# Kernel tuning notes

Measured on AMD Instinct MI355X. Metric: run time of the kernel, lower is better.

Reference implementation:

```python
import jax, jax.numpy as jnp
import numpy as np

B, L, H = 4, 1024, 1024          # docs, seq_len, hidden (LUKE-large)
NH, M, E, R = 16, 64, 24, 512    # attn heads, mentions/doc, entities/doc, pairs/doc
EMB, BLK, NCLS = 768, 64, 97     # embed_size, block_size, num_class


def setup_inputs() -> dict:
    key = jax.random.key(0)
    ks = jax.random.split(key, 10)
    s = 0.02
    return {
        "seq_lhs": jax.random.normal(ks[0], (B, L, H), jnp.float32),
        "ent_lhs": jax.random.normal(ks[1], (B, M, H), jnp.float32),
        "ent_to_seq_attn": jax.random.uniform(ks[2], (B, NH, M, L), jnp.float32),
        "entity_id_labels": jax.random.randint(ks[3], (B, M), 0, E),
        "hts": jax.random.randint(ks[4], (B, R, 2), 0, E),
        "Wh": jax.random.normal(ks[5], (2 * H, EMB), jnp.float32) * s,
        "bh": jnp.zeros((EMB,), jnp.float32),
        "Wt": jax.random.normal(ks[6], (2 * H, EMB), jnp.float32) * s,
        "bt": jnp.zeros((EMB,), jnp.float32),
        "Wb": jax.random.normal(ks[7], (EMB * BLK, 768), jnp.float32) * s,
        "bb": jnp.zeros((768,), jnp.float32),
        "Wc": jax.random.normal(ks[8], (768, NCLS), jnp.float32) * s,
        "bc": jnp.zeros((NCLS,), jnp.float32),
    }


def reference(seq_lhs, ent_lhs, ent_to_seq_attn, entity_id_labels, hts,
              Wh, bh, Wt, bt, Wb, bb, Wc, bc):
    dt = seq_lhs.dtype
    # mention -> entity segment mask [B, E, M]
    mask = entity_id_labels[:, None, :] == jnp.arange(E)[None, :, None]
    counts = mask.sum(-1)  # [B, E]
    # entity embedding: logsumexp over its mentions (== identity for 1 mention),
    # zeros for entities with no mentions
    masked = jnp.where(mask[..., None], ent_lhs[:, None, :, :], jnp.asarray(-1e30, dt))
    ent_emb = jax.scipy.special.logsumexp(masked, axis=2)           # [B, E, H]
    ent_emb = jnp.where((counts > 0)[..., None], ent_emb, jnp.asarray(0.0, dt))
    # entity -> seq attention: mean over mentions, zeros for empty entities
    mf = mask.astype(dt)
    ent_attn = jnp.einsum('bem,bhml->behl', mf, ent_to_seq_attn)    # [B, E, NH, L]
    ent_attn = ent_attn / jnp.maximum(counts, 1)[:, :, None, None].astype(dt)
    # gather per-pair head/tail embeddings and attentions
    h_idx, t_idx = hts[..., 0], hts[..., 1]                          # [B, R]
    hs = jnp.take_along_axis(ent_emb, h_idx[..., None], axis=1)      # [B, R, H]
    ts = jnp.take_along_axis(ent_emb, t_idx[..., None], axis=1)
    ha = jnp.take_along_axis(ent_attn, h_idx[..., None, None], axis=1)  # [B, R, NH, L]
    ta = jnp.take_along_axis(ent_attn, t_idx[..., None, None], axis=1)
    ht = (ha * ta).mean(2)                                           # [B, R, L]
    ht = ht / (ht.sum(-1, keepdims=True) + 1e-5)
    rel = jnp.einsum('bld,brl->brd', seq_lhs, ht)                    # [B, R, H]
    # head/tail extractors with context concat
    he = jnp.tanh(jnp.concatenate([hs, rel], -1) @ Wh + bh)          # [B, R, EMB]
    te = jnp.tanh(jnp.concatenate([ts, rel], -1) @ Wt + bt)
    K = EMB // BLK
    b1 = he.reshape(B * R, K, BLK)
    b2 = te.reshape(B * R, K, BLK)
    bl = (b1[:, :, :, None] * b2[:, :, None, :]).reshape(B * R, EMB * BLK)
    embeds = bl @ Wb + bb                                            # [B*R, 768]
    return embeds @ Wc + bc                                          # [B*R, NCLS]
```

## Files before the change

kernel.cpp:

```cpp
#include <hip/hip_runtime.h>
#include <stdint.h>
#include <math.h>

#define B_    4
#define L_    1024
#define H_    1024
#define NH_   16
#define M_    64
#define E_    24
#define R_    512
#define EMB_  768
#define BLK_  64
#define NCLS_ 97
#define NR_   2048
#define KBIG_ 49152

typedef unsigned short ushort_t;
typedef unsigned int uint_t;
typedef short bf16x8 __attribute__((ext_vector_type(8)));
typedef float f32x4  __attribute__((ext_vector_type(4)));
typedef __bf16 bf16v2 __attribute__((ext_vector_type(2)));

__device__ __forceinline__ float bf2f(ushort_t u) {
    return __uint_as_float(((unsigned)u) << 16);
}
__device__ __forceinline__ ushort_t f2bf_rne(float f) {
    unsigned u = __float_as_uint(f);
    return (ushort_t)((u + 0x7fffu + ((u >> 16) & 1u)) >> 16);
}
__device__ __forceinline__ void cp16(const void* g, void* l) {
    __builtin_amdgcn_global_load_lds(
        (const __attribute__((address_space(1))) void*)g,
        (__attribute__((address_space(3))) void*)l, 16, 0, 0);
}

__global__ __launch_bounds__(256) void k_transpose_cvt(
    const float* __restrict__ in, ushort_t* __restrict__ out, int rows, int cols)
{
    __shared__ float t[64][65];
    int batch = blockIdx.z;
    in  += (size_t)batch * rows * cols;
    out += (size_t)batch * rows * cols;
    int c0 = blockIdx.x * 64, r0 = blockIdx.y * 64;
    int tx = threadIdx.x & 63, ty = threadIdx.x >> 6;
#pragma unroll
    for (int dr = 0; dr < 64; dr += 4)
        t[dr + ty][tx] = in[(size_t)(r0 + dr + ty) * cols + (c0 + tx)];
    __syncthreads();
    int c = threadIdx.x >> 2;
    int rk = (threadIdx.x & 3) * 16;
    ushort_t us[16];
#pragma unroll
    for (int q = 0; q < 16; q++) us[q] = f2bf_rne(t[rk + q][c]);
    ushort_t* op = &out[(size_t)(c0 + c) * rows + r0 + rk];
    *reinterpret_cast<int4*>(op)     = *reinterpret_cast<const int4*>(&us[0]);
    *reinterpret_cast<int4*>(op + 8) = *reinterpret_cast<const int4*>(&us[8]);
}

__global__ __launch_bounds__(256) void k_ent_emb(
    const float* __restrict__ ent_lhs, const int* __restrict__ labels,
    float* __restrict__ ent_emb)
{
    int b = blockIdx.x / E_, e = blockIdx.x % E_;
    __shared__ int list[M_];
    __shared__ int cnt;
    if (threadIdx.x == 0) cnt = 0;
    __syncthreads();
    if (threadIdx.x < M_ && labels[b * M_ + threadIdx.x] == e) {
        int p = atomicAdd(&cnt, 1);
        list[p] = threadIdx.x;
    }
    __syncthreads();
    int n = cnt;
    const float* base = ent_lhs + (size_t)b * M_ * H_;
    float* outp = ent_emb + ((size_t)b * E_ + e) * H_;
    for (int h = threadIdx.x; h < H_; h += blockDim.x) {
        if (n == 0) { outp[h] = 0.f; continue; }
        float mx = -1e30f;
        for (int i = 0; i < n; i++) mx = fmaxf(mx, base[(size_t)list[i] * H_ + h]);
        float s = 0.f;
        for (int i = 0; i < n; i++) s += __expf(base[(size_t)list[i] * H_ + h] - mx);
        outp[h] = mx + __logf(s);
    }
}

__global__ __launch_bounds__(256) void k_ent_attn(
    const float* __restrict__ attn, const int* __restrict__ labels,
    float* __restrict__ ent_attn)
{
    int idx = blockIdx.x;
    int nh = idx % NH_;
    int be = idx / NH_;
    int e = be % E_, b = be / E_;
    __shared__ int list[M_];
    __shared__ int cnt;
    if (threadIdx.x == 0) cnt = 0;
    __syncthreads();
    if (threadIdx.x < M_ && labels[b * M_ + threadIdx.x] == e) {
        int p = atomicAdd(&cnt, 1);
        list[p] = threadIdx.x;
    }
    __syncthreads();
    int n = cnt;
    float inv = 1.f / fmaxf((float)n, 1.f);
    const float* base = attn + ((size_t)b * NH_ + nh) * M_ * L_;
    float* outp = ent_attn + (((size_t)b * E_ + e) * NH_ + nh) * L_;
    for (int l = threadIdx.x; l < L_; l += blockDim.x) {
        float s = 0.f;
        for (int i = 0; i < n; i++) s += base[(size_t)list[i] * L_ + l];
        outp[l] = s * inv;
    }
}

__global__ __launch_bounds__(256) void k_ht(
    const float* __restrict__ ent_attn, const int* __restrict__ hts,
    ushort_t* __restrict__ ht_bf)
{
    int b = blockIdx.x / R_, r = blockIdx.x % R_;
    int h = hts[((size_t)b * R_ + r) * 2 + 0];
    int t = hts[((size_t)b * R_ + r) * 2 + 1];
    const float* ha = ent_attn + ((size_t)b * E_ + h) * NH_ * L_;
    const float* ta = ent_attn + ((size_t)b * E_ + t) * NH_ * L_;
    float vals[4];
    float local = 0.f;
#pragma unroll
    for (int p = 0; p < 4; p++) {
        int l = threadIdx.x + p * 256;
        float s = 0.f;
#pragma unroll
        for (int nh = 0; nh < NH_; nh++) s += ha[nh * L_ + l] * ta[nh * L_ + l];
        s *= (1.f / NH_);
        vals[p] = s;
        local += s;
    }
    __shared__ float red[4];
    float s = local;
#pragma unroll
    for (int off = 32; off > 0; off >>= 1) s += __shfl_down(s, off, 64);
    if ((threadIdx.x & 63) == 0) red[threadIdx.x >> 6] = s;
    __syncthreads();
    float tot = red[0] + red[1] + red[2] + red[3];
    float inv = 1.f / (tot + 1e-5f);
    ushort_t* outp = ht_bf + ((size_t)b * R_ + r) * L_;
#pragma unroll
    for (int p = 0; p < 4; p++) {
        int l = threadIdx.x + p * 256;
        outp[l] = f2bf_rne(vals[p] * inv);
    }
}

__global__ __launch_bounds__(256) void k_gather(
    const float* __restrict__ ent_emb, const int* __restrict__ hts,
    ushort_t* __restrict__ A1, ushort_t* __restrict__ A2)
{
    int n = blockIdx.x;
    int b = n / R_, r = n % R_;
    int h = hts[((size_t)b * R_ + r) * 2 + 0];
    int t = hts[((size_t)b * R_ + r) * 2 + 1];
    const float* eh = ent_emb + ((size_t)b * E_ + h) * H_;
    const float* et = ent_emb + ((size_t)b * E_ + t) * H_;
    for (int i = threadIdx.x; i < H_; i += 256) {
        A1[(size_t)n * 2048 + i] = f2bf_rne(eh[i]);
        A2[(size_t)n * 2048 + i] = f2bf_rne(et[i]);
    }
}

template <bool BIAS, bool TANH, bool DUAL>
__global__ __launch_bounds__(256) void k_gemm(
    const ushort_t* __restrict__ A, long sA, int lda,
    const ushort_t* __restrict__ Bt, long sB, int ldb,
    int K,
    const float* __restrict__ bias0, const float* __restrict__ bias1,
    ushort_t* __restrict__ C0, ushort_t* __restrict__ C1, long sC, int ldc)
{
    __shared__ ushort_t smem[2 * 128 * 72];
    ushort_t* As = smem;
    ushort_t* Bs = smem + 128 * 72;
    const int tid = threadIdx.x;
    const int lane = tid & 63, wid = tid >> 6;
    const int wr = wid >> 1, wc = wid & 1;
    const int z = blockIdx.z;
    const int m0 = blockIdx.y * 128, n0 = blockIdx.x * 128;
    A  += (long)z * sA;
    Bt += (long)z * sB;

    const f32x4 zero = {0.f, 0.f, 0.f, 0.f};
    f32x4 acc[4][4];
#pragma unroll
    for (int i = 0; i < 4; i++)
#pragma unroll
        for (int j = 0; j < 4; j++) acc[i][j] = zero;

    const int mrow = wr * 64 + (lane & 15);
    const int nrow = wc * 64 + (lane & 15);
    const int koff = (lane >> 4) * 8;

    for (int k0 = 0; k0 < K; k0 += 64) {
        __syncthreads();
#pragma unroll
        for (int p = 0; p < 4; p++) {
            int idx = tid + p * 256;
            int row = idx >> 3, seg = idx & 7;
            *reinterpret_cast<int4*>(&As[row * 72 + seg * 8]) =
                *reinterpret_cast<const int4*>(&A[(long)(m0 + row) * lda + k0 + seg * 8]);
            *reinterpret_cast<int4*>(&Bs[row * 72 + seg * 8]) =
                *reinterpret_cast<const int4*>(&Bt[(long)(n0 + row) * ldb + k0 + seg * 8]);
        }
        __syncthreads();
#pragma unroll
        for (int ks = 0; ks < 2; ks++) {
            bf16x8 af[4], bfg[4];
#pragma unroll
            for (int mt = 0; mt < 4; mt++)
                af[mt] = *reinterpret_cast<const bf16x8*>(&As[(mrow + mt * 16) * 72 + ks * 32 + koff]);
#pragma unroll
            for (int nt = 0; nt < 4; nt++)
                bfg[nt] = *reinterpret_cast<const bf16x8*>(&Bs[(nrow + nt * 16) * 72 + ks * 32 + koff]);
#pragma unroll
            for (int mt = 0; mt < 4; mt++)
#pragma unroll
                for (int nt = 0; nt < 4; nt++)
                    acc[mt][nt] = __builtin_amdgcn_mfma_f32_16x16x32_bf16(
                        af[mt], bfg[nt], acc[mt][nt], 0, 0, 0);
        }
    }

    const float* bias = BIAS ? (z ? bias1 : bias0) : nullptr;
    __syncthreads();
#pragma unroll
    for (int mt = 0; mt < 4; mt++) {
#pragma unroll
        for (int nt = 0; nt < 4; nt++) {
#pragma unroll
            for (int rg = 0; rg < 4; rg++) {
                int row = wr * 64 + mt * 16 + (lane >> 4) * 4 + rg;
                int col = wc * 64 + nt * 16 + (lane & 15);
                float v = acc[mt][nt][rg];
                if (BIAS) v += bias[n0 + col];
                if (TANH) {
                    float vc = fminf(fmaxf(v, -15.f), 15.f);
                    float ex = __expf(2.f * vc);
                    v = (ex - 1.f) / (ex + 1.f);
                }
                smem[row * 132 + col] = f2bf_rne(v);
            }
        }
    }
    __syncthreads();
    {
        int row = tid >> 1, half = tid & 1;
        const ushort_t* src = &smem[row * 132 + half * 64];
        ushort_t* dst0 = &C0[(long)z * sC + (long)(m0 + row) * ldc + n0 + half * 64];
#pragma unroll
        for (int q = 0; q < 8; q++)
            *reinterpret_cast<int4*>(dst0 + q * 8) = *reinterpret_cast<const int4*>(src + q * 8);
        if (DUAL) {
            ushort_t* dst1 = &C1[(long)z * sC + (long)(m0 + row) * ldc + n0 + half * 64];
#pragma unroll
            for (int q = 0; q < 8; q++)
                *reinterpret_cast<int4*>(dst1 + q * 8) = *reinterpret_cast<const int4*>(src + q * 8);
        }
    }
}

__global__ __launch_bounds__(256, 3) void k_bilinear(
    const ushort_t* __restrict__ he, const ushort_t* __restrict__ te,
    const ushort_t* __restrict__ Wbt, float* __restrict__ embedsN, int slices)
{
    __shared__ ushort_t HEs[128 * 72];
    __shared__ ushort_t Bsh[128 * 64];
    const int tid = threadIdx.x;
    const int lane = tid & 63, wid = tid >> 6;
    const int wr = wid >> 1, wc = wid & 1;
    const int bid = blockIdx.x;
    const int z = bid & 7;
    const int w = bid >> 3;
    const int d0 = (w % 6) * 128, n0 = (w / 6) * 128;
    const int c0 = z * 96, cend = c0 + 96;

    const f32x4 zero = {0.f, 0.f, 0.f, 0.f};
    f32x4 acc[4][4];
#pragma unroll
    for (int i = 0; i < 4; i++)
#pragma unroll
        for (int j = 0; j < 4; j++) acc[i][j] = zero;

    const int r15 = lane & 15;
    const int q4 = lane >> 4;
    const int mrow = wr * 64 + r15;
    const int koff = q4 * 8;

    const ushort_t* Pg = Wbt
        + (long)(d0 + wid * 32 + (lane >> 3)) * KBIG_
        + ((lane & 7) ^ ((lane >> 3) & 7)) * 8;
    ushort_t* Pl = Bsh + wid * 2048;

    int c = c0;
    while (c < cend) {
        const int kk = c >> 6;
        const int i0 = c & 63;
        const int i1 = min(64, i0 + (cend - c));

        __syncthreads();
#pragma unroll
        for (int p = 0; p < 4; p++) {
            int idx = tid + p * 256;
            int row = idx >> 3, seg = idx & 7;
            *reinterpret_cast<int4*>(&HEs[row * 72 + seg * 8]) =
                *reinterpret_cast<const int4*>(&he[(long)(n0 + row) * EMB_ + kk * 64 + seg * 8]);
        }
        __syncthreads();

        uint4 tef[4][2];
#pragma unroll
        for (int mt = 0; mt < 4; mt++)
#pragma unroll
            for (int ks = 0; ks < 2; ks++)
                tef[mt][ks] = *reinterpret_cast<const uint4*>(
                    &te[(long)(n0 + mrow + mt * 16) * EMB_ + kk * 64 + ks * 32 + koff]);

        for (int i = i0; i < i1; i++) {
            const ushort_t* g = Pg + (long)(kk * 64 + i) * 64;
            cp16(g,              Pl);
            cp16(g +  8 * KBIG_, Pl + 512);
            cp16(g + 16 * KBIG_, Pl + 1024);
            cp16(g + 24 * KBIG_, Pl + 1536);
            __syncthreads();

#pragma unroll
            for (int ks = 0; ks < 2; ks++) {
                const int segoff = (((ks * 4 + q4) ^ (r15 & 7)) * 8);
                bf16x8 bfr[4];
#pragma unroll
                for (int nt = 0; nt < 4; nt++)
                    bfr[nt] = *reinterpret_cast<const bf16x8*>(
                        &Bsh[(wc * 64 + nt * 16 + r15) * 64 + segoff]);
#pragma unroll
                for (int mt = 0; mt < 4; mt++) {
                    union { ushort_t s[2]; bf16v2 v; } hu;
                    ushort_t hb = HEs[(mrow + mt * 16) * 72 + i];
                    hu.s[0] = hb; hu.s[1] = hb;
                    union U { uint4 q; bf16v2 p[4]; bf16x8 v; };
                    U t, a;
                    t.q = tef[mt][ks];
#pragma unroll
                    for (int qq = 0; qq < 4; qq++) a.p[qq] = t.p[qq] * hu.v;
#pragma unroll
                    for (int nt = 0; nt < 4; nt++)
                        acc[mt][nt] = __builtin_amdgcn_mfma_f32_16x16x32_bf16(
                            a.v, bfr[nt], acc[mt][nt], 0, 0, 0);
                }
            }
            __syncthreads();
        }
        c += (i1 - i0);
    }

    float* outp = embedsN + (slices == 8 ? (long)z * NR_ * EMB_ : 0l);
    const bool plain = (slices == 8);
#pragma unroll
    for (int mt = 0; mt < 4; mt++)
#pragma unroll
        for (int nt = 0; nt < 4; nt++)
#pragma unroll
            for (int rg = 0; rg < 4; rg++) {
                int n = n0 + wr * 64 + mt * 16 + q4 * 4 + rg;
                int d = d0 + wc * 64 + nt * 16 + r15;
                if (plain) outp[(long)n * EMB_ + d] = acc[mt][nt][rg];
                else       atomicAdd(&outp[(long)n * EMB_ + d], acc[mt][nt][rg]);
            }
}

__global__ __launch_bounds__(128) void k_final(
    const float* __restrict__ embedsN, int nz, const float* __restrict__ bb,
    const float* __restrict__ Wc, const float* __restrict__ bc,
    float* __restrict__ out)
{
    int n = blockIdx.x;
    __shared__ float row[EMB_];
    for (int i = threadIdx.x; i < EMB_; i += 128) {
        float s = bb[i];
        for (int zz = 0; zz < nz; zz++)
            s += embedsN[(size_t)zz * NR_ * EMB_ + (size_t)n * EMB_ + i];
        row[i] = s;
    }
    __syncthreads();
    int j = threadIdx.x;
    if (j < NCLS_) {
        float s = bc[j];
#pragma unroll 8
        for (int d = 0; d < EMB_; d++) s += row[d] * Wc[d * NCLS_ + j];
        out[(size_t)n * NCLS_ + j] = s;
    }
}

extern "C" void kernel_launch(void* const* d_in, const int* in_sizes, int n_in,
                              void* d_out, int out_size, void* d_ws, size_t ws_size,
                              hipStream_t stream)
{
    (void)in_sizes; (void)n_in; (void)out_size;
    const float* seq    = (const float*)d_in[0];
    const float* entl   = (const float*)d_in[1];
    const float* attn   = (const float*)d_in[2];
    const int*   labels = (const int*)d_in[3];
    const int*   hts    = (const int*)d_in[4];
    const float* Wh     = (const float*)d_in[5];
    const float* bh     = (const float*)d_in[6];
    const float* Wt     = (const float*)d_in[7];
    const float* bt     = (const float*)d_in[8];
    const float* Wb     = (const float*)d_in[9];
    const float* bb     = (const float*)d_in[10];
    const float* Wc     = (const float*)d_in[11];
    const float* bc     = (const float*)d_in[12];
    float* out = (float*)d_out;

    char* ws = (char*)d_ws;
    size_t off = 0;
    auto alloc = [&](size_t bytes) -> char* {
        char* p = ws + off;
        off += (bytes + 255) & ~(size_t)255;
        return p;
    };
    float*    ent_emb  = (float*)alloc((size_t)B_ * E_ * H_ * 4);
    float*    ent_attn = (float*)alloc((size_t)B_ * E_ * NH_ * L_ * 4);
    ushort_t* ht_bf    = (ushort_t*)alloc((size_t)B_ * R_ * L_ * 2);
    ushort_t* seq_t    = (ushort_t*)alloc((size_t)B_ * H_ * L_ * 2);
    ushort_t* A1       = (ushort_t*)alloc((size_t)NR_ * 2048 * 2);
    ushort_t* A2       = (ushort_t*)alloc((size_t)NR_ * 2048 * 2);
    ushort_t* Whb      = (ushort_t*)alloc((size_t)EMB_ * 2048 * 2);
    ushort_t* Wtb      = (ushort_t*)alloc((size_t)EMB_ * 2048 * 2);
    ushort_t* he_bf    = (ushort_t*)alloc((size_t)NR_ * EMB_ * 2);
    ushort_t* te_bf    = (ushort_t*)alloc((size_t)NR_ * EMB_ * 2);
    ushort_t* Wbt      = (ushort_t*)alloc((size_t)EMB_ * KBIG_ * 2);

    const size_t slice_b = (size_t)NR_ * EMB_ * 4;
    int slices = (ws_size >= off + 8 * slice_b) ? 8 : 1;
    float* embedsN = (float*)alloc((size_t)slices * slice_b);

    k_transpose_cvt<<<dim3(H_ / 64, L_ / 64, B_), 256, 0, stream>>>(seq, seq_t, L_, H_);
    k_transpose_cvt<<<dim3(EMB_ / 64, 2048 / 64, 1), 256, 0, stream>>>(Wh, Whb, 2048, EMB_);
    k_transpose_cvt<<<dim3(EMB_ / 64, 2048 / 64, 1), 256, 0, stream>>>(Wt, Wtb, 2048, EMB_);
    k_transpose_cvt<<<dim3(EMB_ / 64, KBIG_ / 64, 1), 256, 0, stream>>>(Wb, Wbt, KBIG_, EMB_);

    k_ent_emb<<<B_ * E_, 256, 0, stream>>>(entl, labels, ent_emb);
    k_ent_attn<<<B_ * E_ * NH_, 256, 0, stream>>>(attn, labels, ent_attn);

    k_ht<<<NR_, 256, 0, stream>>>(ent_attn, hts, ht_bf);
    k_gather<<<NR_, 256, 0, stream>>>(ent_emb, hts, A1, A2);

    k_gemm<false, false, true><<<dim3(H_ / 128, R_ / 128, B_), 256, 0, stream>>>(
        ht_bf, (long)R_ * L_, L_,
        seq_t, (long)H_ * L_, L_,
        L_, nullptr, nullptr,
        A1 + 1024, A2 + 1024, (long)R_ * 2048, 2048);

    k_gemm<true, true, false><<<dim3(EMB_ / 128, NR_ / 128, 2), 256, 0, stream>>>(
        A1, (long)NR_ * 2048, 2048,
        Whb, (long)EMB_ * 2048, 2048,
        2048, bh, bt,
        he_bf, nullptr, (long)NR_ * EMB_, EMB_);

    if (slices == 1)
        (void)hipMemsetAsync(embedsN, 0, slice_b, stream);
    k_bilinear<<<768, 256, 0, stream>>>(he_bf, te_bf, Wbt, embedsN, slices);

    k_final<<<NR_, 128, 0, stream>>>(embedsN, slices, bb, Wc, bc, out);
}
```

Measured before the change: 634.7 us.

## Double-buffer Wb tiles in bilinear kernel and compute outer product in fp32

Splits the shared Wb tile buffer into two halves so the async copy for step i+1 is issued before computing step i, with explicit vmcnt waits and raw barriers replacing __syncthreads. The te fragment is pre-converted to fp32 and the he*te product is formed in fp32 then rounded to bf16, instead of a packed bf16 multiply. This aims to hide global-load latency behind MFMA work. In exchange it doubles LDS use, which may lower occupancy at launch_bounds(256,3), and adds more VALU conversion work and registers per step.

```diff
diff --git a/kernel.cpp b/kernel.cpp
--- a/kernel.cpp
+++ b/kernel.cpp
@@ -268,7 +268,7 @@
     const ushort_t* __restrict__ Wbt, float* __restrict__ embedsN, int slices)
 {
     __shared__ ushort_t HEs[128 * 72];
-    __shared__ ushort_t Bsh[128 * 64];
+    __shared__ ushort_t Bsh[2][128 * 64];
     const int tid = threadIdx.x;
     const int lane = tid & 63, wid = tid >> 6;
     const int wr = wid >> 1, wc = wid & 1;
@@ -293,7 +293,6 @@
     const ushort_t* Pg = Wbt
         + (long)(d0 + wid * 32 + (lane >> 3)) * KBIG_
         + ((lane & 7) ^ ((lane >> 3) & 7)) * 8;
-    ushort_t* Pl = Bsh + wid * 2048;
 
     int c = c0;
     while (c < cend) {
@@ -302,6 +301,16 @@
         const int i1 = min(64, i0 + (cend - c));
 
         __syncthreads();
+
+        {
+            const ushort_t* g = Pg + (long)(kk * 64 + i0) * 64;
+            ushort_t* Pl = Bsh[0] + wid * 2048;
+            cp16(g,              Pl);
+            cp16(g +  8 * KBIG_, Pl + 512);
+            cp16(g + 16 * KBIG_, Pl + 1024);
+            cp16(g + 24 * KBIG_, Pl + 1536);
+        }
+
 #pragma unroll
         for (int p = 0; p < 4; p++) {
             int idx = tid + p * 256;
@@ -311,47 +320,62 @@
         }
         __syncthreads();
 
-        uint4 tef[4][2];
+        float tf[4][2][8];
 #pragma unroll
         for (int mt = 0; mt < 4; mt++)
 #pragma unroll
-            for (int ks = 0; ks < 2; ks++)
-                tef[mt][ks] = *reinterpret_cast<const uint4*>(
+            for (int ks = 0; ks < 2; ks++) {
+                uint4 t = *reinterpret_cast<const uint4*>(
                     &te[(long)(n0 + mrow + mt * 16) * EMB_ + kk * 64 + ks * 32 + koff]);
-
+                const ushort_t* ts = reinterpret_cast<const ushort_t*>(&t);
+#pragma unroll
+                for (int qq = 0; qq < 8; qq++) tf[mt][ks][qq] = bf2f(ts[qq]);
+            }
+
+        int cur = 0;
         for (int i = i0; i < i1; i++) {
-            const ushort_t* g = Pg + (long)(kk * 64 + i) * 64;
-            cp16(g,              Pl);
-            cp16(g +  8 * KBIG_, Pl + 512);
-            cp16(g + 16 * KBIG_, Pl + 1024);
-            cp16(g + 24 * KBIG_, Pl + 1536);
-            __syncthreads();
-
+            if (i + 1 < i1) {
+                const ushort_t* g = Pg + (long)(kk * 64 + i + 1) * 64;
+                ushort_t* Pl = Bsh[cur ^ 1] + wid * 2048;
+                cp16(g,              Pl);
+                cp16(g +  8 * KBIG_, Pl + 512);
+                cp16(g + 16 * KBIG_, Pl + 1024);
+                cp16(g + 24 * KBIG_, Pl + 1536);
+                asm volatile("s_waitcnt vmcnt(4)" ::: "memory");
+            } else {
+                asm volatile("s_waitcnt vmcnt(0)" ::: "memory");
+            }
+            __builtin_amdgcn_s_barrier();
+            __builtin_amdgcn_sched_barrier(0);
+
+            const ushort_t* Bcur = Bsh[cur];
+            bf16x8 bfr[2][4];
 #pragma unroll
             for (int ks = 0; ks < 2; ks++) {
                 const int segoff = (((ks * 4 + q4) ^ (r15 & 7)) * 8);
-                bf16x8 bfr[4];
 #pragma unroll
                 for (int nt = 0; nt < 4; nt++)
-                    bfr[nt] = *reinterpret_cast<const bf16x8*>(
-                        &Bsh[(wc * 64 + nt * 16 + r15) * 64 + segoff]);
-#pragma unroll
-                for (int mt = 0; mt < 4; mt++) {
-                    union { ushort_t s[2]; bf16v2 v; } hu;
-                    ushort_t hb = HEs[(mrow + mt * 16) * 72 + i];
-                    hu.s[0] = hb; hu.s[1] = hb;
-                    union U { uint4 q; bf16v2 p[4]; bf16x8 v; };
-                    U t, a;
-                    t.q = tef[mt][ks];
-#pragma unroll
-                    for (int qq = 0; qq < 4; qq++) a.p[qq] = t.p[qq] * hu.v;
+                    bfr[ks][nt] = *reinterpret_cast<const bf16x8*>(
+                        &Bcur[(wc * 64 + nt * 16 + r15) * 64 + segoff]);
+            }
+#pragma unroll
+            for (int mt = 0; mt < 4; mt++) {
+                float hf = bf2f(HEs[(mrow + mt * 16) * 72 + i]);
+#pragma unroll
+                for (int ks = 0; ks < 2; ks++) {
+                    union { __bf16 h[8]; bf16x8 v; } af;
+#pragma unroll
+                    for (int qq = 0; qq < 8; qq++)
+                        af.h[qq] = (__bf16)(tf[mt][ks][qq] * hf);
 #pragma unroll
                     for (int nt = 0; nt < 4; nt++)
                         acc[mt][nt] = __builtin_amdgcn_mfma_f32_16x16x32_bf16(
-                            a.v, bfr[nt], acc[mt][nt], 0, 0, 0);
+                            af.v, bfr[ks][nt], acc[mt][nt], 0, 0, 0);
                 }
             }
-            __syncthreads();
+            __builtin_amdgcn_s_barrier();
+            __builtin_amdgcn_sched_barrier(0);
+            cur ^= 1;
         }
         c += (i1 - i0);
     }
```

Measured after the change: 636.9 us. Within noise of the previous version (+0.3%).

## Retile bilinear kernel to 256x96 with triple-buffered async Wb loads

Applied to the files above, without the earlier changes.

Reshapes the bilinear GEMM kernel to 512-thread blocks covering 256 rows by 96 output columns, with 512 blocks instead of 768. Wb tiles now stream through a three-stage LDS ring buffer. The first four waves issue async copies two iterations ahead, gated by vmcnt waits and a single barrier per step instead of two. The he tile is stored with an XOR swizzle instead of padding. This is meant to hide global load latency and cut barrier stalls, at the cost of more LDS per block and fragile hand-written waitcnt synchronisation.

```diff
diff --git a/kernel.cpp b/kernel.cpp
--- a/kernel.cpp
+++ b/kernel.cpp
@@ -263,37 +263,37 @@
     }
 }
 
-__global__ __launch_bounds__(256, 3) void k_bilinear(
+__global__ __launch_bounds__(512, 4) void k_bilinear(
     const ushort_t* __restrict__ he, const ushort_t* __restrict__ te,
     const ushort_t* __restrict__ Wbt, float* __restrict__ embedsN, int slices)
 {
-    __shared__ ushort_t HEs[128 * 72];
-    __shared__ ushort_t Bsh[128 * 64];
+    __shared__ ushort_t HEs[256 * 64];
+    __shared__ ushort_t Bsh[3 * 96 * 64];
     const int tid = threadIdx.x;
     const int lane = tid & 63, wid = tid >> 6;
-    const int wr = wid >> 1, wc = wid & 1;
+    const int wn = wid >> 1, wd = wid & 1;
     const int bid = blockIdx.x;
     const int z = bid & 7;
     const int w = bid >> 3;
-    const int d0 = (w % 6) * 128, n0 = (w / 6) * 128;
+    const int d0 = (w & 7) * 96, n0 = (w >> 3) * 256;
     const int c0 = z * 96, cend = c0 + 96;
 
     const f32x4 zero = {0.f, 0.f, 0.f, 0.f};
-    f32x4 acc[4][4];
+    f32x4 acc[4][3];
 #pragma unroll
     for (int i = 0; i < 4; i++)
 #pragma unroll
-        for (int j = 0; j < 4; j++) acc[i][j] = zero;
+        for (int j = 0; j < 3; j++) acc[i][j] = zero;
 
     const int r15 = lane & 15;
     const int q4 = lane >> 4;
-    const int mrow = wr * 64 + r15;
+    const int mrow = wn * 64 + r15;
     const int koff = q4 * 8;
+    const int hswz = (r15 & 7) << 3;
 
     const ushort_t* Pg = Wbt
-        + (long)(d0 + wid * 32 + (lane >> 3)) * KBIG_
+        + (long)(d0 + wid * 8 + (lane >> 3)) * KBIG_
         + ((lane & 7) ^ ((lane >> 3) & 7)) * 8;
-    ushort_t* Pl = Bsh + wid * 2048;
 
     int c = c0;
     while (c < cend) {
@@ -302,14 +302,6 @@
         const int i1 = min(64, i0 + (cend - c));
 
         __syncthreads();
-#pragma unroll
-        for (int p = 0; p < 4; p++) {
-            int idx = tid + p * 256;
-            int row = idx >> 3, seg = idx & 7;
-            *reinterpret_cast<int4*>(&HEs[row * 72 + seg * 8]) =
-                *reinterpret_cast<const int4*>(&he[(long)(n0 + row) * EMB_ + kk * 64 + seg * 8]);
-        }
-        __syncthreads();
 
         uint4 tef[4][2];
 #pragma unroll
@@ -319,39 +311,75 @@
                 tef[mt][ks] = *reinterpret_cast<const uint4*>(
                     &te[(long)(n0 + mrow + mt * 16) * EMB_ + kk * 64 + ks * 32 + koff]);
 
+#pragma unroll
+        for (int p = 0; p < 4; p++) {
+            int idx = tid + p * 512;
+            int row = idx >> 3, seg = idx & 7;
+            *reinterpret_cast<int4*>(&HEs[row * 64 + ((seg ^ (row & 7)) * 8)]) =
+                *reinterpret_cast<const int4*>(&he[(long)(n0 + row) * EMB_ + kk * 64 + seg * 8]);
+        }
+
+        if (wid < 4) {
+#pragma unroll
+            for (int tb = 0; tb < 2; tb++) {
+                const ushort_t* g = Pg + (long)(kk * 64 + i0 + tb) * 64;
+                char* Pl = (char*)Bsh + tb * 12288 + wid * 1024;
+                cp16(g,                   Pl);
+                cp16(g + 32 * (long)KBIG_, Pl + 4096);
+                cp16(g + 64 * (long)KBIG_, Pl + 8192);
+            }
+        }
+        asm volatile("s_waitcnt lgkmcnt(0)" ::: "memory");
+
+        int rd = 0;
         for (int i = i0; i < i1; i++) {
-            const ushort_t* g = Pg + (long)(kk * 64 + i) * 64;
-            cp16(g,              Pl);
-            cp16(g +  8 * KBIG_, Pl + 512);
-            cp16(g + 16 * KBIG_, Pl + 1024);
-            cp16(g + 24 * KBIG_, Pl + 1536);
-            __syncthreads();
-
+            if (i + 1 < i1) {
+                if (wid < 4)
+                    asm volatile("s_waitcnt vmcnt(3)" ::: "memory");
+            } else {
+                asm volatile("s_waitcnt vmcnt(0)" ::: "memory");
+            }
+            __builtin_amdgcn_s_barrier();
+            __builtin_amdgcn_sched_barrier(0);
+
+            if (i + 2 < i1 && wid < 4) {
+                const ushort_t* g = Pg + (long)(kk * 64 + i + 2) * 64;
+                char* Pl = (char*)Bsh + ((rd >= 1) ? (rd - 1) : 2) * 12288 + wid * 1024;
+                cp16(g,                   Pl);
+                cp16(g + 32 * (long)KBIG_, Pl + 4096);
+                cp16(g + 64 * (long)KBIG_, Pl + 8192);
+            }
+
+            const ushort_t* Bcur = Bsh + rd * 6144;
+            bf16x8 bfr[2][3];
 #pragma unroll
             for (int ks = 0; ks < 2; ks++) {
                 const int segoff = (((ks * 4 + q4) ^ (r15 & 7)) * 8);
-                bf16x8 bfr[4];
-#pragma unroll
-                for (int nt = 0; nt < 4; nt++)
-                    bfr[nt] = *reinterpret_cast<const bf16x8*>(
-                        &Bsh[(wc * 64 + nt * 16 + r15) * 64 + segoff]);
-#pragma unroll
-                for (int mt = 0; mt < 4; mt++) {
-                    union { ushort_t s[2]; bf16v2 v; } hu;
-                    ushort_t hb = HEs[(mrow + mt * 16) * 72 + i];
-                    hu.s[0] = hb; hu.s[1] = hb;
+#pragma unroll
+                for (int nt = 0; nt < 3; nt++)
+                    bfr[ks][nt] = *reinterpret_cast<const bf16x8*>(
+                        &Bcur[(wd * 48 + nt * 16 + r15) * 64 + segoff]);
+            }
+            const int icol = i ^ hswz;
+#pragma unroll
+            for (int mt = 0; mt < 4; mt++) {
+                union { ushort_t s[2]; bf16v2 v; } hu;
+                ushort_t hb = HEs[(mrow + mt * 16) * 64 + icol];
+                hu.s[0] = hb; hu.s[1] = hb;
+#pragma unroll
+                for (int ks = 0; ks < 2; ks++) {
                     union U { uint4 q; bf16v2 p[4]; bf16x8 v; };
                     U t, a;
                     t.q = tef[mt][ks];
 #pragma unroll
                     for (int qq = 0; qq < 4; qq++) a.p[qq] = t.p[qq] * hu.v;
 #pragma unroll
-                    for (int nt = 0; nt < 4; nt++)
+                    for (int nt = 0; nt < 3; nt++)
                         acc[mt][nt] = __builtin_amdgcn_mfma_f32_16x16x32_bf16(
-                            a.v, bfr[nt], acc[mt][nt], 0, 0, 0);
+                            a.v, bfr[ks][nt], acc[mt][nt], 0, 0, 0);
                 }
             }
-            __syncthreads();
+            rd = (rd == 2) ? 0 : rd + 1;
         }
         c += (i1 - i0);
     }
@@ -361,11 +389,11 @@
 #pragma unroll
     for (int mt = 0; mt < 4; mt++)
 #pragma unroll
-        for (int nt = 0; nt < 4; nt++)
+        for (int nt = 0; nt < 3; nt++)
 #pragma unroll
             for (int rg = 0; rg < 4; rg++) {
-                int n = n0 + wr * 64 + mt * 16 + q4 * 4 + rg;
-                int d = d0 + wc * 64 + nt * 16 + r15;
+                int n = n0 + wn * 64 + mt * 16 + q4 * 4 + rg;
+                int d = d0 + wd * 48 + nt * 16 + r15;
                 if (plain) outp[(long)n * EMB_ + d] = acc[mt][nt][rg];
                 else       atomicAdd(&outp[(long)n * EMB_ + d], acc[mt][nt][rg]);
             }
@@ -462,7 +490,7 @@
 
     if (slices == 1)
         (void)hipMemsetAsync(embedsN, 0, slice_b, stream);
-    k_bilinear<<<768, 256, 0, stream>>>(he_bf, te_bf, Wbt, embedsN, slices);
+    k_bilinear<<<512, 512, 0, stream>>>(he_bf, te_bf, Wbt, embedsN, slices);
 
     k_final<<<NR_, 128, 0, stream>>>(embedsN, slices, bb, Wc, bc, out);
 }
```

New measurement: 640.1 us. No clear change (+0.8%).
